# Kernel tuning notes

Measured on AMD Instinct MI355X. Metric: run time of the kernel, lower is better.

Reference implementation:

```python
import jax, jax.numpy as jnp
import numpy as np

B, N, E = 1024, 4096, 16384
MAX_COL_W, ROW_W = 4, 8


def setup_inputs() -> dict:
    key = jax.random.key(0)
    k1, k2, k3, k4, k5 = jax.random.split(key, 5)
    return {
        "channelLLR": jax.random.normal(k1, (B, N), dtype=jnp.float32),
        "e2oLLR": jax.random.normal(k2, (B, E), dtype=jnp.float32),
        "maxColWeight": MAX_COL_W,
        "edgeToVar": jax.random.randint(k3, (B, N, MAX_COL_W), 0, E, dtype=jnp.int32),
        "edgeToVarMask": jnp.ones((B, N, MAX_COL_W), dtype=jnp.float32),
        "oddToEven": jax.random.randint(k4, (B, E), 0, N, dtype=jnp.int32),
        "edgeToChk": jax.random.randint(k5, (B, E, ROW_W - 1), 0, E, dtype=jnp.int32),
        "rowWeight": ROW_W,
        "alpha": jnp.ones((1,), dtype=jnp.float32),
    }


def reference(channelLLR, e2oLLR, maxColWeight, edgeToVar, edgeToVarMask,
              oddToEven, edgeToChk, rowWeight, alpha):
    b = channelLLR.shape[0]
    # variable-node update: gather incoming edge messages, mask, sum
    msgToVars = jnp.take_along_axis(e2oLLR, edgeToVar.reshape(b, -1), axis=1)
    msgToVars = msgToVars.reshape(b, -1, maxColWeight) * edgeToVarMask  # [B,N,colW]
    llr = channelLLR + jnp.sum(msgToVars, axis=2)                      # [B,N]
    # extrinsic variable-to-check message per edge
    llr = jnp.take_along_axis(llr, oddToEven, axis=1) - e2oLLR         # [B,E]
    # check-node min-sum update over rowWeight-1 peer edges
    msgToChecks = jnp.take_along_axis(llr, edgeToChk.reshape(b, -1), axis=1)
    msgToChecks = msgToChecks.reshape(b, -1, rowWeight - 1)            # [B,E,rowW-1]
    mn = jnp.min(jnp.abs(msgToChecks), axis=2)                         # [B,E]
    sign = jnp.prod(jnp.sign(msgToChecks), axis=2)                     # [B,E]
    e2o = sign * (mn * alpha[0])                                       # [B,E]
    # marginalized posterior LLR per variable node
    out = jnp.take_along_axis(e2o, edgeToVar.reshape(b, -1), axis=1)
    out = out.reshape(b, -1, maxColWeight) * edgeToVarMask
    out = channelLLR + jnp.sum(out, axis=2)                            # [B,N]
    return (out, e2o)
```

## Files before the change

kernel.cpp:

```cpp
#include <hip/hip_runtime.h>

#define BB   1024
#define NN   4096
#define EE   16384
#define COLW 4
#define ROWW1 7
#define TPB  512

__global__ __launch_bounds__(TPB, 4) void msl_fused_kernel(
    const float* __restrict__ channelLLR,
    const float* __restrict__ e2oLLR,
    const int*   __restrict__ edgeToVar,
    const float* __restrict__ edgeToVarMask,
    const int*   __restrict__ oddToEven,
    const int*   __restrict__ edgeToChk,
    const float* __restrict__ alpha,
    float*       __restrict__ out,
    float*       __restrict__ e2o_out)
{
    __shared__ __align__(16) float llr_lds[NN];
    __shared__ __align__(16) float edge_lds[EE];
    const int b   = blockIdx.x;
    const int tid = threadIdx.x;
    const float alph = alpha[0];

    {
        const float4* __restrict__ src = reinterpret_cast<const float4*>(e2oLLR + (size_t)b * EE);
        float4* dst = reinterpret_cast<float4*>(edge_lds);
        #pragma unroll
        for (int k = 0; k < EE / 4 / TPB; ++k) {
            int i = tid + k * TPB;
            dst[i] = src[i];
        }
    }
    __syncthreads();

    int4   idxreg[NN / TPB];
    float4 mreg[NN / TPB];
    {
        const int4*   __restrict__ ev4 = reinterpret_cast<const int4*>(edgeToVar + (size_t)b * NN * COLW);
        const float4* __restrict__ mk4 = reinterpret_cast<const float4*>(edgeToVarMask + (size_t)b * NN * COLW);
        const float*  __restrict__ chrow = channelLLR + (size_t)b * NN;
        #pragma unroll
        for (int k = 0; k < NN / TPB; ++k) {
            int n = tid + k * TPB;
            int4  idx = ev4[n];
            float4 m  = mk4[n];
            float acc = chrow[n];
            acc += edge_lds[idx.x] * m.x;
            acc += edge_lds[idx.y] * m.y;
            acc += edge_lds[idx.z] * m.z;
            acc += edge_lds[idx.w] * m.w;
            llr_lds[n] = acc;
            idxreg[k] = idx; mreg[k] = m;
        }
    }
    __syncthreads();

    {
        const int* __restrict__ o2erow = oddToEven + (size_t)b * EE;
        #pragma unroll 8
        for (int k = 0; k < EE / TPB; ++k) {
            int e = tid + k * TPB;
            int o = o2erow[e];
            float v = llr_lds[o] - edge_lds[e];
            edge_lds[e] = v;
        }
    }
    __syncthreads();

    float e2oreg[EE / TPB];
    {
        const int* __restrict__ ecrow = edgeToChk + (size_t)b * EE * ROWW1;
        float* __restrict__ e2orow = e2o_out + (size_t)b * EE;
        #pragma unroll
        for (int k = 0; k < EE / TPB; ++k) {
            int e = tid + k * TPB;
            const int* __restrict__ p = ecrow + (size_t)e * ROWW1;
            float mn = 3.0e38f;
            unsigned sgn = 0u;
            #pragma unroll
            for (int j = 0; j < ROWW1; ++j) {
                float v = edge_lds[p[j]];
                sgn ^= __float_as_uint(v);
                mn = fminf(mn, fabsf(v));
            }
            float val = mn * alph;
            float r = __uint_as_float(__float_as_uint(val) ^ (sgn & 0x80000000u));
            e2oreg[k] = r;
            e2orow[e] = r;
        }
    }
    __syncthreads();

    #pragma unroll
    for (int k = 0; k < EE / TPB; ++k) {
        edge_lds[tid + k * TPB] = e2oreg[k];
    }
    __syncthreads();

    {
        float* __restrict__ outrow = out + (size_t)b * NN;
        const float* __restrict__ chrow = channelLLR + (size_t)b * NN;
        #pragma unroll
        for (int k = 0; k < NN / TPB; ++k) {
            int n = tid + k * TPB;
            int4  idx = idxreg[k];
            float4 m  = mreg[k];
            float acc = chrow[n];
            acc += edge_lds[idx.x] * m.x;
            acc += edge_lds[idx.y] * m.y;
            acc += edge_lds[idx.z] * m.z;
            acc += edge_lds[idx.w] * m.w;
            outrow[n] = acc;
        }
    }
}

extern "C" void kernel_launch(void* const* d_in, const int* in_sizes, int n_in,
                              void* d_out, int out_size, void* d_ws, size_t ws_size,
                              hipStream_t stream) {
    const float* channelLLR    = (const float*)d_in[0];
    const float* e2oLLR        = (const float*)d_in[1];
    const int*   edgeToVar     = (const int*)d_in[3];
    const float* edgeToVarMask = (const float*)d_in[4];
    const int*   oddToEven     = (const int*)d_in[5];
    const int*   edgeToChk     = (const int*)d_in[6];
    const float* alpha         = (const float*)d_in[8];

    float* out     = (float*)d_out;
    float* e2o_out = (float*)d_out + (size_t)BB * NN;

    msl_fused_kernel<<<BB, TPB, 0, stream>>>(
        channelLLR, e2oLLR, edgeToVar, edgeToVarMask,
        oddToEven, edgeToChk, alpha, out, e2o_out);
}
```

Before: 178.3 us.

## Coalesce check-node index loads through an LDS transpose with register prefetch

In the check-node phase, each wave now reads its 64 edges' seven edgeToChk indices as contiguous, coalesced chunks. It gathers the corresponding edge values into a double-buffered per-wave LDS scratch, then each lane reads back its own seven values at stride 7. Indices for the next group are prefetched into registers while the current group is gathered. The block size doubles to 1024 threads and the llr buffer is reused as scratch, so LDS use goes up. This trades the old strided per-thread index reads for extra LDS traffic and wave-level waits.

New measurement: 166.7 us. 6.5% less time.

```diff
diff --git a/kernel.cpp b/kernel.cpp
--- a/kernel.cpp
+++ b/kernel.cpp
@@ -5,9 +5,12 @@
 #define EE   16384
 #define COLW 4
 #define ROWW1 7
-#define TPB  512
+#define TPB  1024
+#define NWAVE (TPB / 64)
+#define GRP_DW (64 * ROWW1)
+#define SCR_DW (NWAVE * GRP_DW)
 
-__global__ __launch_bounds__(TPB, 4) void msl_fused_kernel(
+__global__ __launch_bounds__(TPB) void msl_fused_kernel(
     const float* __restrict__ channelLLR,
     const float* __restrict__ e2oLLR,
     const int*   __restrict__ edgeToVar,
@@ -18,10 +21,12 @@
     float*       __restrict__ out,
     float*       __restrict__ e2o_out)
 {
-    __shared__ __align__(16) float llr_lds[NN];
+    __shared__ __align__(16) float scr_lds[2 * SCR_DW];
     __shared__ __align__(16) float edge_lds[EE];
-    const int b   = blockIdx.x;
-    const int tid = threadIdx.x;
+    const int b    = blockIdx.x;
+    const int tid  = threadIdx.x;
+    const int wave = tid >> 6;
+    const int lane = tid & 63;
     const float alph = alpha[0];
 
     {
@@ -51,7 +56,7 @@
             acc += edge_lds[idx.y] * m.y;
             acc += edge_lds[idx.z] * m.z;
             acc += edge_lds[idx.w] * m.w;
-            llr_lds[n] = acc;
+            scr_lds[n] = acc;
             idxreg[k] = idx; mreg[k] = m;
         }
     }
@@ -63,7 +68,7 @@
         for (int k = 0; k < EE / TPB; ++k) {
             int e = tid + k * TPB;
             int o = o2erow[e];
-            float v = llr_lds[o] - edge_lds[e];
+            float v = scr_lds[o] - edge_lds[e];
             edge_lds[e] = v;
         }
     }
@@ -71,24 +76,41 @@
 
     float e2oreg[EE / TPB];
     {
-        const int* __restrict__ ecrow = edgeToChk + (size_t)b * EE * ROWW1;
+        const int* __restrict__ ecrow = edgeToChk + (size_t)b * (size_t)EE * ROWW1;
         float* __restrict__ e2orow = e2o_out + (size_t)b * EE;
+        int idx[ROWW1];
+        {
+            const int* __restrict__ p = ecrow + (size_t)wave * GRP_DW + lane;
+            #pragma unroll
+            for (int j = 0; j < ROWW1; ++j) idx[j] = p[64 * j];
+        }
         #pragma unroll
-        for (int k = 0; k < EE / TPB; ++k) {
-            int e = tid + k * TPB;
-            const int* __restrict__ p = ecrow + (size_t)e * ROWW1;
+        for (int it = 0; it < EE / TPB; ++it) {
+            const int g = it * NWAVE + wave;
+            float* __restrict__ scratch = scr_lds + (it & 1) * SCR_DW + wave * GRP_DW;
+            #pragma unroll
+            for (int j = 0; j < ROWW1; ++j) scratch[lane + 64 * j] = edge_lds[idx[j]];
+            if (it + 1 < EE / TPB) {
+                const int* __restrict__ p = ecrow + (size_t)(g + NWAVE) * GRP_DW + lane;
+                #pragma unroll
+                for (int j = 0; j < ROWW1; ++j) idx[j] = p[64 * j];
+            }
+            __builtin_amdgcn_wave_barrier();
+            asm volatile("s_waitcnt lgkmcnt(0)" ::: "memory");
+            __builtin_amdgcn_wave_barrier();
             float mn = 3.0e38f;
             unsigned sgn = 0u;
+            const float* __restrict__ sb = scratch + lane * ROWW1;
             #pragma unroll
             for (int j = 0; j < ROWW1; ++j) {
-                float v = edge_lds[p[j]];
-                sgn ^= __float_as_uint(v);
-                mn = fminf(mn, fabsf(v));
+                float u = sb[j];
+                sgn ^= __float_as_uint(u);
+                mn = fminf(mn, fabsf(u));
             }
             float val = mn * alph;
             float r = __uint_as_float(__float_as_uint(val) ^ (sgn & 0x80000000u));
-            e2oreg[k] = r;
-            e2orow[e] = r;
+            e2oreg[it] = r;
+            e2orow[64 * g + lane] = r;
         }
     }
     __syncthreads();
```
